# Kernel tuning notes

Hardware: AMD Instinct MI355X
Metric: run time of the kernel (lower is better)

The kernel has to match this reference:

```python
import jax, jax.numpy as jnp
import numpy as np

F_BINS = 12
T_STEPS = 15
N = F_BINS * T_STEPS  # 180 patches
C = 768
R = C // 4            # 192 reduced dim for Q/K
B = 256
LN_EPS = 1e-5


def _build_physical_adjacency():
    A = np.zeros((N, N), dtype=np.float32)
    for f in range(F_BINS):
        for t in range(T_STEPS):
            i = f * T_STEPS + t
            if t < T_STEPS - 1:
                j = f * T_STEPS + (t + 1)
                A[i, j] = 1.0
                A[j, i] = 1.0
            hf = f * 2 + 1
            if hf < F_BINS:
                j = hf * T_STEPS + t
                A[i, j] = 1.0
                A[j, i] = 1.0
    A = A / (A.sum(axis=1, keepdims=True) + 1e-8)
    return jnp.asarray(A)


def setup_inputs() -> dict:
    key = jax.random.key(0)
    ks = jax.random.split(key, 8)
    x = jax.random.normal(ks[0], (B, N, C), dtype=jnp.float32)
    Wq = jax.random.normal(ks[1], (C, R), dtype=jnp.float32) * 0.02
    bq = jnp.zeros((R,), dtype=jnp.float32)
    Wk = jax.random.normal(ks[2], (C, R), dtype=jnp.float32) * 0.02
    bk = jnp.zeros((R,), dtype=jnp.float32)
    Wg = jax.random.normal(ks[3], (C, C), dtype=jnp.float32) * 0.02
    bg = jnp.zeros((C,), dtype=jnp.float32)
    gamma = jnp.ones((C,), dtype=jnp.float32)
    beta = jnp.zeros((C,), dtype=jnp.float32)
    alpha = jnp.asarray(0.8, dtype=jnp.float32)
    A_phys = _build_physical_adjacency()
    return {"x": x, "Wq": Wq, "bq": bq, "Wk": Wk, "bk": bk,
            "Wg": Wg, "bg": bg, "gamma": gamma, "beta": beta,
            "alpha": alpha, "A_phys": A_phys}


def reference(x, Wq, bq, Wk, bk, Wg, bg, gamma, beta, alpha, A_phys):
    # Q/K projections: [B,N,R]
    Q = jnp.einsum('bnc,cr->bnr', x, Wq) + bq
    K = jnp.einsum('bnc,cr->bnr', x, Wk) + bk
    # Dynamic adjacency: scaled dot-product softmax over nodes.
    scores = jnp.einsum('bnr,bmr->bnm', Q, K) / jnp.sqrt(jnp.asarray(R, x.dtype))
    A_dyn = jax.nn.softmax(scores, axis=-1)  # dropout is identity in eval
    a = jax.nn.sigmoid(alpha)
    A_comb = a * A_phys[None, :, :] + (1.0 - a) * A_dyn
    # GCN aggregation + projection
    z = jnp.einsum('bnm,bmc->bnc', A_comb, x)
    z = jnp.einsum('bnc,cd->bnd', z, Wg) + bg
    h = x + jax.nn.relu(z)
    # LayerNorm over channel dim
    mu = jnp.mean(h, axis=-1, keepdims=True)
    var = jnp.mean((h - mu) ** 2, axis=-1, keepdims=True)
    out = (h - mu) * jax.lax.rsqrt(var + LN_EPS) * gamma + beta
    return out
```

## Files before the change

kernel.cpp:

```cpp
#include <hip/hip_runtime.h>
#include <hip/hip_bf16.h>
#include <math.h>
#include <stdint.h>

#define BB   256
#define NN   180
#define CC   768
#define RR   192
#define MROWS (BB*NN)
#define KPAD 192

typedef __attribute__((ext_vector_type(8))) __bf16 bf16x8;
typedef __attribute__((ext_vector_type(4))) __bf16 bf16x4;
typedef __attribute__((ext_vector_type(4))) float  floatx4;

__device__ __forceinline__ void gload_lds16(const __bf16* g, __bf16* lds)
{
    __builtin_amdgcn_global_load_lds(
        (const __attribute__((address_space(1))) void*)(uintptr_t)(const void*)g,
        (__attribute__((address_space(3))) void*)(uintptr_t)(void*)lds,
        16, 0, 0);
}

template<int MODE>
__global__ __launch_bounds__(256) void gemm128(
    const __bf16* __restrict__ A,  int lda, long sAb,
    const __bf16* __restrict__ Bt, int ldb, long sBb,
    void* __restrict__ Cout, int ldc, long sCb,
    int M, int N, int K,
    const float* __restrict__ bias,
    const float* __restrict__ scale,
    const float* __restrict__ addx)
{
    const int z = blockIdx.z;
    const __bf16* Ab = A  + (long)z * sAb;
    const __bf16* Bb = Bt + (long)z * sBb;
    const int m0 = blockIdx.y * 128;
    const int n0 = blockIdx.x * 128;
    const int t  = threadIdx.x;
    const int w  = t >> 6;
    const int l  = t & 63;
    const int lr = l & 15;
    const int q  = l >> 4;

    __shared__ __align__(16) __bf16 sa[2][128 * 32];
    __shared__ __align__(16) __bf16 sb[2][128 * 32];

    floatx4 acc[4][4] = {};

    const int wm = (w & 1) * 64;
    const int wn = (w >> 1) * 64;

    const int srow = l >> 2;
    const int skc  = (l & 3) * 8;

    int arow0 = m0 + w * 16 + srow;        if (arow0 > M - 1) arow0 = M - 1;
    int arow1 = m0 + (w + 4) * 16 + srow;  if (arow1 > M - 1) arow1 = M - 1;
    int brow0 = n0 + w * 16 + srow;        if (brow0 > N - 1) brow0 = N - 1;
    int brow1 = n0 + (w + 4) * 16 + srow;  if (brow1 > N - 1) brow1 = N - 1;

    const __bf16* agp0 = Ab + (long)arow0 * lda + skc;
    const __bf16* agp1 = Ab + (long)arow1 * lda + skc;
    const __bf16* bgp0 = Bb + (long)brow0 * ldb + skc;
    const __bf16* bgp1 = Bb + (long)brow1 * ldb + skc;

    auto issue = [&](int buf, int k0) {
        gload_lds16(agp0 + k0, &sa[buf][(size_t)w * 512]);
        gload_lds16(agp1 + k0, &sa[buf][(size_t)(w + 4) * 512]);
        gload_lds16(bgp0 + k0, &sb[buf][(size_t)w * 512]);
        gload_lds16(bgp1 + k0, &sb[buf][(size_t)(w + 4) * 512]);
    };

    auto compute = [&](int buf) {
        bf16x8 af[4], bfv[4];
#pragma unroll
        for (int i = 0; i < 4; ++i)
            af[i] = *reinterpret_cast<const bf16x8*>(&sa[buf][(wm + i * 16 + lr) * 32 + q * 8]);
#pragma unroll
        for (int j = 0; j < 4; ++j)
            bfv[j] = *reinterpret_cast<const bf16x8*>(&sb[buf][(wn + j * 16 + lr) * 32 + q * 8]);
#pragma unroll
        for (int i = 0; i < 4; ++i)
#pragma unroll
            for (int j = 0; j < 4; ++j)
                acc[i][j] = __builtin_amdgcn_mfma_f32_16x16x32_bf16(af[i], bfv[j], acc[i][j], 0, 0, 0);
    };

    issue(0, 0);
    __syncthreads();
    for (int k0 = 0; k0 < K; k0 += 64) {
        issue(1, k0 + 32);
        compute(0);
        __syncthreads();
        if (k0 + 64 < K) issue(0, k0 + 64);
        compute(1);
        __syncthreads();
    }

#pragma unroll
    for (int i = 0; i < 4; ++i) {
        const int mbase = m0 + wm + i * 16 + q * 4;
#pragma unroll
        for (int j = 0; j < 4; ++j) {
            const int n = n0 + wn + j * 16 + lr;
#pragma unroll
            for (int r = 0; r < 4; ++r) {
                const int m = mbase + r;
                if (m < M && n < N) {
                    float v = acc[i][j][r];
                    if (MODE == 0) {
                        v = (v + bias[n]) * scale[n];
                        ((__bf16*)Cout)[(long)z * sCb + (long)m * ldc + n] = (__bf16)v;
                    } else if (MODE == 1) {
                        ((__bf16*)Cout)[(long)z * sCb + (long)m * ldc + n] = (__bf16)v;
                    } else {
                        v = v + bias[n];
                        v = v > 0.f ? v : 0.f;
                        v += addx[(long)m * ldc + n];
                        ((float*)Cout)[(long)m * ldc + n] = v;
                    }
                }
            }
        }
    }
}

__global__ __launch_bounds__(256) void convert_x(const float4* __restrict__ x4,
                                                 __bf16* __restrict__ xb, int n4)
{
    int i = blockIdx.x * 256 + threadIdx.x;
    int stride = gridDim.x * 256;
    for (; i < n4; i += stride) {
        float4 v = x4[i];
        bf16x4 o;
        o[0] = (__bf16)v.x; o[1] = (__bf16)v.y; o[2] = (__bf16)v.z; o[3] = (__bf16)v.w;
        *reinterpret_cast<bf16x4*>(xb + 4 * (long)i) = o;
    }
}

__global__ __launch_bounds__(256) void prep_weights(
    const float* __restrict__ Wq, const float* __restrict__ bq,
    const float* __restrict__ Wk, const float* __restrict__ bk,
    const float* __restrict__ Wg,
    __bf16* __restrict__ WqkT, __bf16* __restrict__ WgT,
    float* __restrict__ biasqk, float* __restrict__ scaleqk)
{
    int blk = blockIdx.x, t = threadIdx.x;
    if (blk < 384) {
        int n = blk;
        const float* W = (n < RR) ? Wq : Wk;
        int nn = (n < RR) ? n : n - RR;
        for (int k = t; k < CC; k += 256)
            WqkT[(long)n * CC + k] = (__bf16)W[(long)k * RR + nn];
        if (blk == 0) {
            for (int i = t; i < 384; i += 256) {
                biasqk[i]  = (i < RR) ? bq[i] : bk[i - RR];
                scaleqk[i] = (i < RR) ? rsqrtf((float)RR) : 1.0f;
            }
        }
    } else {
        int n = blk - 384;
        for (int k = t; k < CC; k += 256)
            WgT[(long)n * CC + k] = (__bf16)Wg[(long)k * CC + n];
    }
}

__global__ __launch_bounds__(256) void transpose_x(const __bf16* __restrict__ xb,
                                                   __bf16* __restrict__ xbT)
{
    const int c0 = (blockIdx.x % 12) * 64;
    const int b  = blockIdx.x / 12;
    __shared__ __bf16 lds[64 * 194];
    const int t = threadIdx.x;

    for (int i = 0; i < 45; ++i) {
        int idx = i * 256 + t;
        int m = idx >> 6, c = idx & 63;
        lds[c * 194 + m] = xb[((long)(b * NN + m)) * CC + c0 + c];
    }
    __syncthreads();
    for (int j = 0; j < 48; ++j) {
        int idx = j * 256 + t;
        int c = idx / KPAD, m = idx % KPAD;
        __bf16 v = (m < NN) ? lds[c * 194 + m] : (__bf16)0.0f;
        xbT[((long)(b * CC + c0 + c)) * KPAD + m] = v;
    }
}

__global__ __launch_bounds__(256) void softmax_combine(
    const __bf16* __restrict__ S, const float* __restrict__ A_phys,
    const float* __restrict__ alpha, __bf16* __restrict__ Acomb)
{
    const int w = threadIdx.x >> 6, l = threadIdx.x & 63;
    const long row = (long)blockIdx.x * 4 + w;
    const int b = (int)(row / NN), n = (int)(row % NN);
    const __bf16* Srow = S + ((long)b * NN + n) * NN;

    float v[3];
#pragma unroll
    for (int i = 0; i < 3; ++i) {
        int m = l + 64 * i;
        v[i] = (m < NN) ? (float)Srow[m] : -1e30f;
    }
    float mx = fmaxf(fmaxf(v[0], v[1]), v[2]);
    for (int off = 32; off; off >>= 1) mx = fmaxf(mx, __shfl_xor(mx, off, 64));

    float e[3], sum = 0.f;
#pragma unroll
    for (int i = 0; i < 3; ++i) {
        int m = l + 64 * i;
        e[i] = (m < NN) ? expf(v[i] - mx) : 0.f;
        sum += e[i];
    }
    for (int off = 32; off; off >>= 1) sum += __shfl_xor(sum, off, 64);

    const float a   = 1.f / (1.f + expf(-alpha[0]));
    const float inv = (1.f - a) / sum;
    __bf16* Orow = Acomb + ((long)b * NN + n) * KPAD;
#pragma unroll
    for (int i = 0; i < 3; ++i) {
        int m = l + 64 * i;
        if (m < KPAD) {
            float o = (m < NN) ? (a * A_phys[n * NN + m] + e[i] * inv) : 0.f;
            Orow[m] = (__bf16)o;
        }
    }
}

__global__ __launch_bounds__(256) void ln_kernel(float* __restrict__ out,
                                                 const float* __restrict__ gamma,
                                                 const float* __restrict__ beta)
{
    float* p = out + (long)blockIdx.x * CC;
    const int t = threadIdx.x, w = t >> 6, l = t & 63;
    float h[3], s = 0.f, s2 = 0.f;
#pragma unroll
    for (int i = 0; i < 3; ++i) {
        h[i] = p[t + 256 * i];
        s += h[i]; s2 += h[i] * h[i];
    }
    for (int off = 32; off; off >>= 1) { s += __shfl_xor(s, off, 64); s2 += __shfl_xor(s2, off, 64); }
    __shared__ float ps[4], ps2[4];
    if (l == 0) { ps[w] = s; ps2[w] = s2; }
    __syncthreads();
    s  = ps[0] + ps[1] + ps[2] + ps[3];
    s2 = ps2[0] + ps2[1] + ps2[2] + ps2[3];
    const float mu  = s * (1.f / CC);
    const float var = s2 * (1.f / CC) - mu * mu;
    const float rs  = rsqrtf(var + 1e-5f);
#pragma unroll
    for (int i = 0; i < 3; ++i) {
        int c = t + 256 * i;
        p[c] = (h[i] - mu) * rs * gamma[c] + beta[c];
    }
}

extern "C" void kernel_launch(void* const* d_in, const int* in_sizes, int n_in,
                              void* d_out, int out_size, void* d_ws, size_t ws_size,
                              hipStream_t stream)
{
    const float* x      = (const float*)d_in[0];
    const float* Wq     = (const float*)d_in[1];
    const float* bq     = (const float*)d_in[2];
    const float* Wk     = (const float*)d_in[3];
    const float* bk     = (const float*)d_in[4];
    const float* Wg     = (const float*)d_in[5];
    const float* bg     = (const float*)d_in[6];
    const float* gamma  = (const float*)d_in[7];
    const float* beta   = (const float*)d_in[8];
    const float* alpha  = (const float*)d_in[9];
    const float* A_phys = (const float*)d_in[10];

    char* w = (char*)d_ws;
    __bf16* xb    = (__bf16*)(w + 0);
    __bf16* zbuf  = xb;
    __bf16* xbT   = (__bf16*)(w + 70778880);
    __bf16* QK    = (__bf16*)(w + 146276352);
    __bf16* Acomb = QK;
    __bf16* S     = (__bf16*)(w + 181665792);
    __bf16* WqkT  = (__bf16*)(w + 198254592);
    __bf16* WgT   = (__bf16*)(w + 198844416);
    float*  biasqk  = (float*)(w + 200024064);
    float*  scaleqk = (float*)(w + 200025600);

    convert_x<<<4096, 256, 0, stream>>>((const float4*)x, xb, MROWS * CC / 4);
    prep_weights<<<384 + CC, 256, 0, stream>>>(Wq, bq, Wk, bk, Wg, WqkT, WgT, biasqk, scaleqk);
    transpose_x<<<BB * 12, 256, 0, stream>>>(xb, xbT);

    gemm128<0><<<dim3(384 / 128, MROWS / 128, 1), 256, 0, stream>>>(
        xb, CC, 0L, WqkT, CC, 0L, QK, 384, 0L,
        MROWS, 384, CC, biasqk, scaleqk, nullptr);

    gemm128<1><<<dim3(2, 2, BB), 256, 0, stream>>>(
        QK, 384, (long)NN * 384, QK + RR, 384, (long)NN * 384,
        S, NN, (long)NN * NN,
        NN, NN, RR, nullptr, nullptr, nullptr);

    softmax_combine<<<MROWS / 4, 256, 0, stream>>>(S, A_phys, alpha, Acomb);

    gemm128<1><<<dim3(CC / 128, 2, BB), 256, 0, stream>>>(
        Acomb, KPAD, (long)NN * KPAD, xbT, KPAD, (long)CC * KPAD,
        zbuf, CC, (long)NN * CC,
        NN, CC, KPAD, nullptr, nullptr, nullptr);

    gemm128<3><<<dim3(CC / 128, MROWS / 128, 1), 256, 0, stream>>>(
        zbuf, CC, 0L, WgT, CC, 0L, d_out, CC, 0L,
        MROWS, CC, CC, bg, nullptr, x);

    ln_kernel<<<MROWS, 256, 0, stream>>>((float*)d_out, gamma, beta);
}
```

Before: 680.2 us.

## Add 256x256 tiled GEMM with multi-stage LDS pipeline for projection GEMMs

```diff
diff --git a/kernel.cpp b/kernel.cpp
--- a/kernel.cpp
+++ b/kernel.cpp
@@ -20,6 +20,144 @@
         (const __attribute__((address_space(1))) void*)(uintptr_t)(const void*)g,
         (__attribute__((address_space(3))) void*)(uintptr_t)(void*)lds,
         16, 0, 0);
+}
+
+template<int MODE>
+__global__ __launch_bounds__(512, 2) void gemm256(
+    const __bf16* __restrict__ A,  int lda,
+    const __bf16* __restrict__ Bt, int ldb,
+    void* __restrict__ Cout, int ldc,
+    int M, int N, int K,
+    const float* __restrict__ bias,
+    const float* __restrict__ scale,
+    const float* __restrict__ addx)
+{
+    extern __shared__ __align__(128) __bf16 smem[];
+    __bf16 (*sA)[8192] = (__bf16 (*)[8192])(smem);
+    __bf16 (*sB)[8192] = (__bf16 (*)[8192])(smem + 32768);
+
+    const int nwg = gridDim.x * gridDim.y;
+    const int lin = blockIdx.y * gridDim.x + blockIdx.x;
+    const int qd = nwg >> 3, rr = nwg & 7, xc = lin & 7, oo = lin >> 3;
+    const int wg = (xc < rr ? xc * (qd + 1) : rr * (qd + 1) + (xc - rr) * qd) + oo;
+    const int n0 = (wg % gridDim.x) * 256;
+    const int m0 = (wg / gridDim.x) * 256;
+
+    const int t  = threadIdx.x;
+    const int w  = t >> 6;
+    const int l  = t & 63;
+    const int lr = l & 15;
+    const int q  = l >> 4;
+    const int wm = w >> 2;
+    const int wn = w & 3;
+    const int xr = (lr >> 1) & 3;
+
+    const int a_base = (wm * 128 + lr) * 32 + ((q ^ xr) * 8);
+    const int b_base = (wn * 64  + lr) * 32 + ((q ^ xr) * 8);
+
+    const int srow = l >> 2;
+    const int slog = (l & 3) ^ ((l >> 3) & 3);
+
+    int ar0 = m0 + w * 32 + srow;       if (ar0 > M - 1) ar0 = M - 1;
+    int ar1 = m0 + w * 32 + 16 + srow;  if (ar1 > M - 1) ar1 = M - 1;
+    int br0 = n0 + w * 32 + srow;       if (br0 > N - 1) br0 = N - 1;
+    int br1 = n0 + w * 32 + 16 + srow;  if (br1 > N - 1) br1 = N - 1;
+
+    const __bf16* pA0 = A  + (long)ar0 * lda + slog * 8;
+    const __bf16* pA1 = A  + (long)ar1 * lda + slog * 8;
+    const __bf16* pB0 = Bt + (long)br0 * ldb + slog * 8;
+    const __bf16* pB1 = Bt + (long)br1 * ldb + slog * 8;
+
+    floatx4 acc[8][4] = {};
+
+#define STAGE_A(RG, T, KH) { const int ko_ = (T) * 64 + (KH) * 32;            \
+        gload_lds16(pA0 + ko_, &sA[RG][w * 1024]);                            \
+        gload_lds16(pA1 + ko_, &sA[RG][w * 1024 + 512]); }
+#define STAGE_B(RG, T, KH) { const int ko_ = (T) * 64 + (KH) * 32;            \
+        gload_lds16(pB0 + ko_, &sB[RG][w * 1024]);                            \
+        gload_lds16(pB1 + ko_, &sB[RG][w * 1024 + 512]); }
+
+#define PHASE(MG, KK, RBUF, STAGE_STMT, DO_VM)                                \
+    {                                                                         \
+        bf16x8 af_[4], bv_[4];                                                \
+        _Pragma("unroll")                                                     \
+        for (int ii = 0; ii < 4; ++ii)                                        \
+            af_[ii] = *reinterpret_cast<const bf16x8*>(                       \
+                &sA[(RBUF) * 2 + (KK)][a_base + ((MG) * 4 + ii) * 512]);      \
+        _Pragma("unroll")                                                     \
+        for (int jj = 0; jj < 4; ++jj)                                        \
+            bv_[jj] = *reinterpret_cast<const bf16x8*>(                       \
+                &sB[(RBUF) * 2 + (KK)][b_base + jj * 512]);                   \
+        STAGE_STMT;                                                           \
+        __builtin_amdgcn_s_barrier();                                         \
+        asm volatile("s_waitcnt lgkmcnt(0)" ::: "memory");                    \
+        __builtin_amdgcn_sched_barrier(0);                                    \
+        __builtin_amdgcn_s_setprio(1);                                        \
+        _Pragma("unroll")                                                     \
+        for (int ii = 0; ii < 4; ++ii)                                        \
+            _Pragma("unroll")                                                 \
+            for (int jj = 0; jj < 4; ++jj)                                    \
+                acc[(MG) * 4 + ii][jj] =                                      \
+                    __builtin_amdgcn_mfma_f32_16x16x32_bf16(                  \
+                        af_[ii], bv_[jj], acc[(MG) * 4 + ii][jj], 0, 0, 0);   \
+        __builtin_amdgcn_s_setprio(0);                                        \
+        if (DO_VM) asm volatile("s_waitcnt vmcnt(8)" ::: "memory");           \
+        __builtin_amdgcn_sched_barrier(0);                                    \
+        __builtin_amdgcn_s_barrier();                                         \
+    }
+
+    const int NT    = K >> 6;
+    const int NITER = NT >> 1;
+
+    STAGE_A(0, 0, 0); STAGE_B(0, 0, 0);
+    STAGE_A(1, 0, 1); STAGE_B(1, 0, 1);
+    STAGE_A(2, 1, 0); STAGE_B(2, 1, 0);
+    asm volatile("s_waitcnt vmcnt(8)" ::: "memory");
+    __builtin_amdgcn_s_barrier();
+
+    for (int it = 0; it < NITER; ++it) {
+        const int t1  = 2 * it + 1;
+        const int tS2 = (2 * it + 2 < NT) ? 2 * it + 2 : NT - 1;
+        const int tS3 = (2 * it + 3 < NT) ? 2 * it + 3 : NT - 1;
+        PHASE(0, 0, 0, STAGE_A(3, t1, 1), 0)
+        PHASE(1, 0, 0, STAGE_B(3, t1, 1), 1)
+        PHASE(0, 1, 0, STAGE_A(0, tS2, 0), 0)
+        PHASE(1, 1, 0, STAGE_B(0, tS2, 0), 1)
+        PHASE(0, 0, 1, STAGE_A(1, tS2, 1), 0)
+        PHASE(1, 0, 1, STAGE_B(1, tS2, 1), 1)
+        PHASE(0, 1, 1, STAGE_A(2, tS3, 0), 0)
+        PHASE(1, 1, 1, STAGE_B(2, tS3, 0), 1)
+    }
+#undef PHASE
+#undef STAGE_A
+#undef STAGE_B
+
+#pragma unroll
+    for (int j = 0; j < 4; ++j) {
+        const int n = n0 + wn * 64 + j * 16 + lr;
+        float bi = 0.f, sc = 1.f;
+        if (n < N) { bi = bias[n]; if (MODE == 0) sc = scale[n]; }
+#pragma unroll
+        for (int i = 0; i < 8; ++i) {
+            const int mbase = m0 + wm * 128 + i * 16 + q * 4;
+#pragma unroll
+            for (int r = 0; r < 4; ++r) {
+                const int m = mbase + r;
+                if (m < M && n < N) {
+                    float v = acc[i][j][r];
+                    if (MODE == 0) {
+                        v = (v + bi) * sc;
+                        ((__bf16*)Cout)[(long)m * ldc + n] = (__bf16)v;
+                    } else {
+                        v = v + bi;
+                        v = v > 0.f ? v : 0.f;
+                        v += addx[(long)m * ldc + n];
+                        ((float*)Cout)[(long)m * ldc + n] = v;
+                    }
+                }
+            }
+        }
+    }
 }
 
 template<int MODE>
@@ -271,6 +409,15 @@
     const float* alpha  = (const float*)d_in[9];
     const float* A_phys = (const float*)d_in[10];
 
+    static bool attr_done = false;
+    if (!attr_done) {
+        auto k0 = gemm256<0>;
+        auto k3 = gemm256<3>;
+        hipFuncSetAttribute((const void*)k0, hipFuncAttributeMaxDynamicSharedMemorySize, 131072);
+        hipFuncSetAttribute((const void*)k3, hipFuncAttributeMaxDynamicSharedMemorySize, 131072);
+        attr_done = true;
+    }
+
     char* w = (char*)d_ws;
     __bf16* xb    = (__bf16*)(w + 0);
     __bf16* zbuf  = xb;
@@ -287,8 +434,8 @@
     prep_weights<<<384 + CC, 256, 0, stream>>>(Wq, bq, Wk, bk, Wg, WqkT, WgT, biasqk, scaleqk);
     transpose_x<<<BB * 12, 256, 0, stream>>>(xb, xbT);
 
-    gemm128<0><<<dim3(384 / 128, MROWS / 128, 1), 256, 0, stream>>>(
-        xb, CC, 0L, WqkT, CC, 0L, QK, 384, 0L,
+    gemm256<0><<<dim3(2, MROWS / 256, 1), 512, 131072, stream>>>(
+        xb, CC, WqkT, CC, QK, 384,
         MROWS, 384, CC, biasqk, scaleqk, nullptr);
 
     gemm128<1><<<dim3(2, 2, BB), 256, 0, stream>>>(
@@ -303,8 +450,8 @@
         zbuf, CC, (long)NN * CC,
         NN, CC, KPAD, nullptr, nullptr, nullptr);
 
-    gemm128<3><<<dim3(CC / 128, MROWS / 128, 1), 256, 0, stream>>>(
-        zbuf, CC, 0L, WgT, CC, 0L, d_out, CC, 0L,
+    gemm256<3><<<dim3(CC / 256, MROWS / 256, 1), 512, 131072, stream>>>(
+        zbuf, CC, WgT, CC, d_out, CC,
         MROWS, CC, CC, bg, nullptr, x);
 
     ln_kernel<<<MROWS, 256, 0, stream>>>((float*)d_out, gamma, beta);
```

After: 767.6 us. 12.9% more time.
